# Performance work log

Measured on AMD Instinct MI355X. Metric: run time of the kernel, lower is better.

## Reference

```python
import jax, jax.numpy as jnp
import numpy as np

DIM = 128
EDGE_FEAT_DIM = 2
N_NODES = 50000
N_EDGES = 600000
EPS = 1e-5


def setup_inputs() -> dict:
    key = jax.random.key(0)
    ks = jax.random.split(key, 16)
    d = DIM
    inp = {}
    inp["x"] = jax.random.normal(ks[0], (N_NODES, d), dtype=jnp.float32)
    inp["edge_index"] = jax.random.randint(ks[1], (2, N_EDGES), 0, N_NODES, dtype=jnp.int32)
    inp["edge_weight_norm"] = jax.random.uniform(ks[2], (N_EDGES,), dtype=jnp.float32)
    inp["edge_feat"] = jax.random.normal(ks[3], (N_EDGES, EDGE_FEAT_DIM), dtype=jnp.float32)
    inp["batch"] = jnp.zeros((N_NODES,), dtype=jnp.int32)
    # phi: Linear(dim, dim)
    inp["W_phi"] = jax.random.normal(ks[4], (d, d), dtype=jnp.float32) * (1.0 / np.sqrt(d))
    inp["b_phi"] = jnp.zeros((d,), dtype=jnp.float32)
    # edge_gate: Linear(2d+2, d) -> BN(d) -> GELU -> Linear(d, 1)
    din = 2 * d + EDGE_FEAT_DIM
    inp["W_g1"] = jax.random.normal(ks[5], (din, d), dtype=jnp.float32) * (1.0 / np.sqrt(din))
    inp["b_g1"] = jnp.zeros((d,), dtype=jnp.float32)
    inp["bn_gamma"] = jnp.ones((d,), dtype=jnp.float32)
    inp["bn_beta"] = jnp.zeros((d,), dtype=jnp.float32)
    inp["bn_mean"] = jnp.zeros((d,), dtype=jnp.float32)
    inp["bn_var"] = jnp.ones((d,), dtype=jnp.float32)
    inp["W_g2"] = jax.random.normal(ks[6], (d, 1), dtype=jnp.float32) * (1.0 / np.sqrt(d))
    inp["b_g2"] = jnp.zeros((1,), dtype=jnp.float32)
    # upd: Linear(2d, d)
    inp["W_u"] = jax.random.normal(ks[7], (2 * d, d), dtype=jnp.float32) * (1.0 / np.sqrt(2 * d))
    inp["b_u"] = jnp.zeros((d,), dtype=jnp.float32)
    # LayerNorm(dim)
    inp["ln_gamma"] = jnp.ones((d,), dtype=jnp.float32)
    inp["ln_beta"] = jnp.zeros((d,), dtype=jnp.float32)
    return inp


def reference(x, edge_index, edge_weight_norm, edge_feat, batch,
              W_phi, b_phi, W_g1, b_g1, bn_gamma, bn_beta, bn_mean, bn_var,
              W_g2, b_g2, W_u, b_u, ln_gamma, ln_beta):
    src, dst = edge_index[0], edge_index[1]
    # phi(x): [N, d]
    xj = x @ W_phi + b_phi
    # edge gate MLP on [x_dst, x_src, e]: [E, 2d+2]
    g_in = jnp.concatenate([x[dst], x[src], edge_feat], axis=-1)
    h1 = g_in @ W_g1 + b_g1
    h1 = (h1 - bn_mean) * jax.lax.rsqrt(bn_var + EPS) * bn_gamma + bn_beta  # BN eval mode
    h1 = jax.nn.gelu(h1, approximate=False)
    gate = jax.nn.sigmoid(h1 @ W_g2 + b_g2)[:, 0]  # [E]
    # messages and scatter-add aggregation
    msg = xj[src] * (edge_weight_norm * gate)[:, None]  # [E, d]
    agg = jax.ops.segment_sum(msg, dst, num_segments=x.shape[0])  # [N, d]
    # update MLP + GELU + residual + LayerNorm
    h = jnp.concatenate([x, agg], axis=-1) @ W_u + b_u
    h = jax.nn.gelu(h, approximate=False)
    y = x + h
    mu = jnp.mean(y, axis=-1, keepdims=True)
    var = jnp.var(y, axis=-1, keepdims=True)
    return (y - mu) * jax.lax.rsqrt(var + EPS) * ln_gamma + ln_beta
```

## Files before the change

### kernel.cpp

```cpp
#include <hip/hip_runtime.h>
#include <hip/hip_fp16.h>
#include <math.h>

#define DIM 128
#define NN 50000
#define NE 600000
#define EPS 1e-5f
#define CAP 64

struct H8 { __half2 h[4]; };
struct F8 { float4 a, b; };

typedef _Float16 f16x8 __attribute__((ext_vector_type(8)));
typedef float    f32x4 __attribute__((ext_vector_type(4)));

__device__ __forceinline__ float gelu_fast(float x) {
    const float c1 = 2.3022085f;
    const float c2 = 0.1029437f;
    const float x2 = x * x;
    const float z  = x * __builtin_fmaf(c2, x2, c1);
    const float u  = __builtin_amdgcn_exp2f(z);
    const float r  = __builtin_amdgcn_rcpf(1.f + u);
    return __builtin_fmaf(-x, r, x);
}

__device__ __forceinline__ float sigmoid_fast(float y) {
    const float u = __builtin_amdgcn_exp2f(-1.4426950409f * y);
    return __builtin_amdgcn_rcpf(1.f + u);
}

__global__ __launch_bounds__(256) void k_prep(
    const float* __restrict__ Wg1, const float* __restrict__ bg1,
    const float* __restrict__ bng, const float* __restrict__ bnb,
    const float* __restrict__ bnm, const float* __restrict__ bnv,
    const float* __restrict__ Wphi, const float* __restrict__ bphi,
    const float* __restrict__ Wu,
    __half* __restrict__ WABth, float* __restrict__ bA,
    float* __restrict__ w0p, float* __restrict__ w1p,
    __half* __restrict__ Wct, float* __restrict__ bpu)
{
    if (blockIdx.x < 128) {
        const int k = blockIdx.x;
        const int t = threadIdx.x;
        const int c = t & 127;
        const float s = bng[c] * rsqrtf(bnv[c] + EPS);
        const float w = (t < 128) ? Wg1[k * DIM + c] : Wg1[(DIM + k) * DIM + c];
        WABth[t * DIM + k] = __float2half(w * s);
        if (k == 0 && t < 128) {
            const float tt = bnb[c] - bnm[c] * s;
            bA[c]  = bg1[c] * s + tt;
            w0p[c] = Wg1[256 * DIM + c] * s;
            w1p[c] = Wg1[257 * DIM + c] * s;
        }
    } else {
        const int a = blockIdx.x - 128;
        const int j = threadIdx.x;
        if (j < 128) {
            float acc = 0.f;
            #pragma unroll 8
            for (int k = 0; k < DIM; ++k)
                acc += Wphi[a * DIM + k] * Wu[(DIM + k) * DIM + j];
            Wct[j * 256 + a]       = __float2half(Wu[a * DIM + j]);
            Wct[j * 256 + 128 + a] = __float2half(acc);
            if (a == 0) {
                float b = 0.f;
                #pragma unroll 8
                for (int k = 0; k < DIM; ++k)
                    b += bphi[k] * Wu[(DIM + k) * DIM + j];
                bpu[j] = b;
            }
        }
    }
}

__global__ __launch_bounds__(256) void k_node_mfma(
    const float* __restrict__ x, const __half* __restrict__ WABth,
    const float* __restrict__ bA,
    __half* __restrict__ A, __half* __restrict__ Bv, __half* __restrict__ xh,
    int* __restrict__ deg)
{
    __shared__ __half xs[64][136];
    __shared__ __half ys[64][136];

    const int t    = threadIdx.x;
    const int wv   = t >> 6;
    const int lane = t & 63;
    const int n16  = lane & 15;
    const int quad = lane >> 4;
    const int m0   = blockIdx.x * 64;

    {
        const int z = blockIdx.x * 256 + t;
        if (z < NN) deg[z] = 0;
    }

    #pragma unroll
    for (int i = 0; i < 4; ++i) {
        const int idx = i * 256 + t;
        const int row = idx >> 4;
        const int col = (idx & 15) * 8;
        const int grow = min(m0 + row, NN - 1);
        const float4 xa = *(const float4*)(x + (size_t)grow * DIM + col);
        const float4 xb = *(const float4*)(x + (size_t)grow * DIM + col + 4);
        f16x8 af;
        af[0] = (_Float16)xa.x; af[1] = (_Float16)xa.y;
        af[2] = (_Float16)xa.z; af[3] = (_Float16)xa.w;
        af[4] = (_Float16)xb.x; af[5] = (_Float16)xb.y;
        af[6] = (_Float16)xb.z; af[7] = (_Float16)xb.w;
        *(f16x8*)&xs[row][col] = af;
        *(f16x8*)(xh + (size_t)grow * DIM + col) = af;
    }
    __syncthreads();

    f32x4 acc[4][4];
    #pragma unroll
    for (int mt = 0; mt < 4; ++mt)
        #pragma unroll
        for (int nt = 0; nt < 4; ++nt)
            acc[mt][nt] = (f32x4){0.f, 0.f, 0.f, 0.f};

    #pragma unroll
    for (int ks = 0; ks < 4; ++ks) {
        const int ko = ks * 32 + quad * 8;
        f16x8 bf[4];
        #pragma unroll
        for (int nt = 0; nt < 4; ++nt) {
            const int c = wv * 64 + nt * 16 + n16;
            bf[nt] = *(const f16x8*)(WABth + c * DIM + ko);
        }
        #pragma unroll
        for (int mt = 0; mt < 4; ++mt) {
            const f16x8 af = *(const f16x8*)&xs[mt * 16 + n16][ko];
            #pragma unroll
            for (int nt = 0; nt < 4; ++nt)
                acc[mt][nt] = __builtin_amdgcn_mfma_f32_16x16x32_f16(
                    af, bf[nt], acc[mt][nt], 0, 0, 0);
        }
    }
    __syncthreads();

    #pragma unroll
    for (int nt = 0; nt < 4; ++nt) {
        const int c = wv * 64 + nt * 16 + n16;
        const float bias = (c < 128) ? bA[c] : 0.f;
        #pragma unroll
        for (int mt = 0; mt < 4; ++mt)
            #pragma unroll
            for (int reg = 0; reg < 4; ++reg) {
                const int row = mt * 16 + quad * 4 + reg;
                const __half hv = __float2half(acc[mt][nt][reg] + bias);
                if (c < 128) xs[row][c]       = hv;
                else         ys[row][c - 128] = hv;
            }
    }
    __syncthreads();

    #pragma unroll
    for (int i = 0; i < 8; ++i) {
        const int chunk = t + i * 256;
        const int row = chunk >> 5;
        const int o   = (chunk & 31) * 8;
        if (m0 + row < NN) {
            if (o < 128) {
                const uint4 v = *(const uint4*)&xs[row][o];
                *(uint4*)(A + (size_t)(m0 + row) * DIM + o) = v;
            } else {
                const uint4 v = *(const uint4*)&ys[row][o - 128];
                *(uint4*)(Bv + (size_t)(m0 + row) * DIM + o - 128) = v;
            }
        }
    }
}

__global__ __launch_bounds__(256) void k_gate(
    const int*   __restrict__ ei,  const float* __restrict__ ew,
    const float* __restrict__ ef,
    const __half* __restrict__ A,  const __half* __restrict__ Bv,
    const float* __restrict__ w0p, const float* __restrict__ w1p,
    const float* __restrict__ Wg2, const float* __restrict__ bg2,
    int* __restrict__ deg, int2* __restrict__ pairs)
{
    const int t    = threadIdx.x;
    const int lane = t & 63;
    const int sub  = lane >> 4;
    const int sl   = lane & 15;
    const int c8   = sl * 8;
    const int e0   = blockIdx.x * 64 + ((t >> 6) * 4 + sub) * 4;

    const F8 WG = *(const F8*)(Wg2 + c8);
    const F8 W0 = *(const F8*)(w0p + c8);
    const F8 W1 = *(const F8*)(w1p + c8);
    const float bg2v = bg2[0];
    const float* w0 = (const float*)&W0;
    const float* w1 = (const float*)&W1;
    const float* wg = (const float*)&WG;

    const int4   srcs = *(const int4*)(ei + e0);
    const int4   dsts = *(const int4*)(ei + NE + e0);
    const float4 efA  = *(const float4*)(ef + 2 * e0);
    const float4 efB  = *(const float4*)(ef + 2 * e0 + 4);
    const float4 ewv  = *(const float4*)(ew + e0);

    const int se[4] = {srcs.x, srcs.y, srcs.z, srcs.w};
    const int de[4] = {dsts.x, dsts.y, dsts.z, dsts.w};
    const float ef0[4] = {efA.x, efA.z, efB.x, efB.z};
    const float ef1[4] = {efA.y, efA.w, efB.y, efB.w};
    const float ewe[4] = {ewv.x, ewv.y, ewv.z, ewv.w};

    H8 av[4], bv[4];
    #pragma unroll
    for (int e = 0; e < 4; ++e) {
        av[e] = *(const H8*)(A  + (size_t)de[e] * DIM + c8);
        bv[e] = *(const H8*)(Bv + (size_t)se[e] * DIM + c8);
    }

    float p[4] = {0.f, 0.f, 0.f, 0.f};
    #pragma unroll
    for (int i = 0; i < 4; ++i) {
        const int c0 = 2 * i, c1 = 2 * i + 1;
        #pragma unroll
        for (int e = 0; e < 4; ++e) {
            const float2 s = __half22float2(__hadd2(av[e].h[i], bv[e].h[i]));
            float h;
            h = s.x + ef0[e] * w0[c0] + ef1[e] * w1[c0];
            p[e] = __builtin_fmaf(gelu_fast(h), wg[c0], p[e]);
            h = s.y + ef0[e] * w0[c1] + ef1[e] * w1[c1];
            p[e] = __builtin_fmaf(gelu_fast(h), wg[c1], p[e]);
        }
    }

    #pragma unroll
    for (int off = 1; off < 16; off <<= 1) {
        #pragma unroll
        for (int e = 0; e < 4; ++e)
            p[e] += __shfl_xor(p[e], off, 64);
    }

    if (sl == 0) {
        #pragma unroll
        for (int e = 0; e < 4; ++e) {
            const float coef = ewe[e] * sigmoid_fast(p[e] + bg2v);
            const int pos = atomicAdd(&deg[de[e]], 1);
            if (pos < CAP)
                pairs[(size_t)de[e] * CAP + pos] =
                    make_int2(se[e], __float_as_int(coef));
        }
    }
}

__global__ __launch_bounds__(128, 3) void k_agg_update(
    const int* __restrict__ deg, const int2* __restrict__ pairs,
    const __half* __restrict__ xh, const __half* __restrict__ Wct,
    const float* __restrict__ bu, const float* __restrict__ bpu,
    const float* __restrict__ lng, const float* __restrict__ lnb,
    float* __restrict__ out)
{
    __shared__ __half xt[16][136];
    __shared__ __half at[2][16][136];
    __shared__ float  sct[2][16];
    __shared__ float  sred_s[2][16];
    __shared__ float  sred_ss[2][16];

    const int t    = threadIdx.x;
    const int w    = t >> 6;
    const int lane = t & 63;
    const int n16  = lane & 15;
    const int quad = lane >> 4;
    const int m0   = blockIdx.x * 16;

    const int slot = quad;
    const int sl   = n16;
    const int c8   = sl * 8;

    int    cnt[4];
    size_t pb[4];
    #pragma unroll
    for (int r = 0; r < 4; ++r) {
        const int lr = r * 4 + slot;
        const int nc = min(m0 + lr, NN - 1);
        const int d  = min(deg[nc], CAP);
        const int h  = ((d + 2) >> 2) << 1;
        const int lo = w ? h : 0;
        const int hi = w ? d : h;
        cnt[r] = hi - lo;
        pb[r]  = (size_t)nc * CAP + lo;
    }

    #pragma unroll
    for (int i = 0; i < 2; ++i) {
        const int idx = i * 128 + t;
        const int row = idx >> 4;
        const int col = (idx & 15) * 8;
        const int grow = min(m0 + row, NN - 1);
        *(f16x8*)&xt[row][col] = *(const f16x8*)(xh + (size_t)grow * DIM + col);
    }

    float acc[4][8];
    float scn[4] = {0.f, 0.f, 0.f, 0.f};
    #pragma unroll
    for (int r = 0; r < 4; ++r)
        #pragma unroll
        for (int i = 0; i < 8; ++i) acc[r][i] = 0.f;

    const int cmax = max(max(cnt[0], cnt[1]), max(cnt[2], cnt[3]));

    for (int jj = 0; jj < cmax; jj += 4) {
        int4 pq0[4], pq1[4];
        #pragma unroll
        for (int r = 0; r < 4; ++r) {
            pq0[r] = *(const int4*)(&pairs[pb[r] + jj]);
            pq1[r] = *(const int4*)(&pairs[pb[r] + jj + 2]);
        }

        int   ix[16];
        float cf[16];
        #pragma unroll
        for (int r = 0; r < 4; ++r) {
            const int q = 4 * r;
            const bool v0 = (jj     < cnt[r]);
            const bool v1 = (jj + 1 < cnt[r]);
            const bool v2 = (jj + 2 < cnt[r]);
            const bool v3 = (jj + 3 < cnt[r]);
            ix[q]     = v0 ? pq0[r].x : 0;
            cf[q]     = v0 ? __int_as_float(pq0[r].y) : 0.f;
            ix[q + 1] = v1 ? pq0[r].z : 0;
            cf[q + 1] = v1 ? __int_as_float(pq0[r].w) : 0.f;
            ix[q + 2] = v2 ? pq1[r].x : 0;
            cf[q + 2] = v2 ? __int_as_float(pq1[r].y) : 0.f;
            ix[q + 3] = v3 ? pq1[r].z : 0;
            cf[q + 3] = v3 ? __int_as_float(pq1[r].w) : 0.f;
        }

        H8 xv[16];
        #pragma unroll
        for (int q = 0; q < 16; ++q)
            xv[q] = *(const H8*)(xh + (size_t)ix[q] * DIM + c8);

        #pragma unroll
        for (int r = 0; r < 4; ++r) {
            #pragma unroll
            for (int k = 0; k < 4; ++k) {
                const int   q = 4 * r + k;
                const float c = cf[q];
                #pragma unroll
                for (int i = 0; i < 4; ++i) {
                    const float2 f = __half22float2(xv[q].h[i]);
                    acc[r][2 * i]     = __builtin_fmaf(c, f.x, acc[r][2 * i]);
                    acc[r][2 * i + 1] = __builtin_fmaf(c, f.y, acc[r][2 * i + 1]);
                }
                scn[r] += c;
            }
        }
    }

    #pragma unroll
    for (int r = 0; r < 4; ++r) {
        const int lr = r * 4 + slot;
        f16x8 hv;
        #pragma unroll
        for (int i = 0; i < 8; ++i) hv[i] = (_Float16)acc[r][i];
        *(f16x8*)&at[w][lr][c8] = hv;
        if (sl == 0) sct[w][lr] = scn[r];
    }
    __syncthreads();

    f32x4 acc2[4];
    #pragma unroll
    for (int nt = 0; nt < 4; ++nt) acc2[nt] = (f32x4){0.f, 0.f, 0.f, 0.f};

    const int rloc = n16;
    #pragma unroll
    for (int ks = 0; ks < 4; ++ks) {
        const int ko = ks * 32 + quad * 8;
        const f16x8 af = *(const f16x8*)&xt[rloc][ko];
        #pragma unroll
        for (int nt = 0; nt < 4; ++nt) {
            const int c = w * 64 + nt * 16 + n16;
            const f16x8 bf = *(const f16x8*)(Wct + c * 256 + ko);
            acc2[nt] = __builtin_amdgcn_mfma_f32_16x16x32_f16(af, bf, acc2[nt], 0, 0, 0);
        }
    }
    #pragma unroll
    for (int half = 0; half < 2; ++half) {
        #pragma unroll
        for (int ks = 0; ks < 4; ++ks) {
            const int ko = ks * 32 + quad * 8;
            const f16x8 af = *(const f16x8*)&at[half][rloc][ko];
            #pragma unroll
            for (int nt = 0; nt < 4; ++nt) {
                const int c = w * 64 + nt * 16 + n16;
                const f16x8 bf = *(const f16x8*)(Wct + c * 256 + 128 + ko);
                acc2[nt] = __builtin_amdgcn_mfma_f32_16x16x32_f16(af, bf, acc2[nt], 0, 0, 0);
            }
        }
    }

    int   rl[4];
    float scv[4];
    #pragma unroll
    for (int reg = 0; reg < 4; ++reg) {
        rl[reg]  = quad * 4 + reg;
        scv[reg] = sct[0][rl[reg]] + sct[1][rl[reg]];
    }

    float yv[4][4];
    float s[4]  = {0.f, 0.f, 0.f, 0.f};
    float ss[4] = {0.f, 0.f, 0.f, 0.f};

    #pragma unroll
    for (int nt = 0; nt < 4; ++nt) {
        const int c = w * 64 + nt * 16 + n16;
        const float buv = bu[c], bpv = bpu[c];
        #pragma unroll
        for (int reg = 0; reg < 4; ++reg) {
            float h = acc2[nt][reg] + buv + scv[reg] * bpv;
            h = gelu_fast(h);
            const float xv = __half2float(xt[rl[reg]][c]);
            const float y = xv + h;
            yv[nt][reg] = y;
            s[reg]  += y;
            ss[reg] += y * y;
        }
    }

    #pragma unroll
    for (int reg = 0; reg < 4; ++reg) {
        #pragma unroll
        for (int off = 1; off < 16; off <<= 1) {
            s[reg]  += __shfl_xor(s[reg],  off, 64);
            ss[reg] += __shfl_xor(ss[reg], off, 64);
        }
    }
    if (n16 == 0) {
        #pragma unroll
        for (int reg = 0; reg < 4; ++reg) {
            sred_s[w][rl[reg]]  = s[reg];
            sred_ss[w][rl[reg]] = ss[reg];
        }
    }
    __syncthreads();

    float mu[4], rs[4];
    #pragma unroll
    for (int reg = 0; reg < 4; ++reg) {
        const float stot  = sred_s[0][rl[reg]]  + sred_s[1][rl[reg]];
        const float sstot = sred_ss[0][rl[reg]] + sred_ss[1][rl[reg]];
        mu[reg] = stot * (1.f / DIM);
        const float var = sstot * (1.f / DIM) - mu[reg] * mu[reg];
        rs[reg] = rsqrtf(var + EPS);
    }

    #pragma unroll
    for (int nt = 0; nt < 4; ++nt) {
        const int c = w * 64 + nt * 16 + n16;
        const float gg = lng[c], bb2 = lnb[c];
        #pragma unroll
        for (int reg = 0; reg < 4; ++reg) {
            const int grow = m0 + rl[reg];
            if (grow < NN)
                __builtin_nontemporal_store(
                    (yv[nt][reg] - mu[reg]) * rs[reg] * gg + bb2,
                    &out[(size_t)grow * DIM + c]);
        }
    }
}

extern "C" void kernel_launch(void* const* d_in, const int* in_sizes, int n_in,
                              void* d_out, int out_size, void* d_ws, size_t ws_size,
                              hipStream_t stream)
{
    const float* x    = (const float*)d_in[0];
    const int*   ei   = (const int*)  d_in[1];
    const float* ew   = (const float*)d_in[2];
    const float* ef   = (const float*)d_in[3];
    const float* Wphi = (const float*)d_in[5];
    const float* bphi = (const float*)d_in[6];
    const float* Wg1  = (const float*)d_in[7];
    const float* bg1  = (const float*)d_in[8];
    const float* bng  = (const float*)d_in[9];
    const float* bnb  = (const float*)d_in[10];
    const float* bnm  = (const float*)d_in[11];
    const float* bnv  = (const float*)d_in[12];
    const float* Wg2  = (const float*)d_in[13];
    const float* bg2  = (const float*)d_in[14];
    const float* Wu   = (const float*)d_in[15];
    const float* bu   = (const float*)d_in[16];
    const float* lng  = (const float*)d_in[17];
    const float* lnb  = (const float*)d_in[18];

    float* out = (float*)d_out;

    char* wsb = (char*)d_ws;
    size_t off = 0;
    auto carve = [&](size_t bytes) -> void* {
        void* p = wsb + off;
        off += (bytes + 255) & ~(size_t)255;
        return p;
    };
    __half* xh    = (__half*)carve((size_t)NN * DIM * 2);
    __half* A     = (__half*)carve((size_t)NN * DIM * 2);
    __half* Bv    = (__half*)carve((size_t)NN * DIM * 2);
    __half* WABth = (__half*)carve(256 * DIM * 2);
    __half* Wct   = (__half*)carve(DIM * 256 * 2);
    float*  bA    = (float*) carve(DIM * 4);
    float*  w0p   = (float*) carve(DIM * 4);
    float*  w1p   = (float*) carve(DIM * 4);
    float*  bpu   = (float*) carve(DIM * 4);
    int*    deg   = (int*)   carve((size_t)NN * 4);
    int2*   pairs = (int2*)  carve((size_t)NN * CAP * 8 + 256);

    k_prep<<<256, 256, 0, stream>>>(Wg1, bg1, bng, bnb, bnm, bnv,
                                    Wphi, bphi, Wu,
                                    WABth, bA, w0p, w1p, Wct, bpu);
    k_node_mfma<<<(NN + 63) / 64, 256, 0, stream>>>(x, WABth, bA, A, Bv, xh,
                                                    deg);
    k_gate<<<NE / 64, 256, 0, stream>>>(ei, ew, ef, A, Bv, w0p, w1p, Wg2, bg2,
                                        deg, pairs);
    k_agg_update<<<(NN + 15) / 16, 128, 0, stream>>>(deg, pairs, xh, Wct,
                                                     bu, bpu, lng, lnb, out);
}
```

Baseline: 251.8 us.

## Split fused aggregate-update kernel into separate gather and MFMA update kernels

Splits the fused aggregation+update kernel into two kernels. The first is a small gather kernel with one wave per block handling four nodes, each looping over its own degree in chunks of 16 edges. It writes the fp16 aggregate and coefficient sum to a global buffer. The second kernel loads those buffers and performs the MFMA update, GELU and LayerNorm. This is meant to cut the load imbalance and low occupancy of the fused kernel's gather phase, at the cost of an extra global round-trip for the aggregate (about 12.8MB written and read) and one more kernel launch.

Result: slower. 262.7 us (+4.3%).

```diff
diff --git a/kernel.cpp b/kernel.cpp
--- a/kernel.cpp
+++ b/kernel.cpp
@@ -248,16 +248,81 @@
     }
 }
 
-__global__ __launch_bounds__(128, 3) void k_agg_update(
+__global__ __launch_bounds__(64) void k_agg(
     const int* __restrict__ deg, const int2* __restrict__ pairs,
-    const __half* __restrict__ xh, const __half* __restrict__ Wct,
+    const __half* __restrict__ xh,
+    __half* __restrict__ at_g, float* __restrict__ sc_g)
+{
+    const int t    = threadIdx.x;
+    const int slot = t >> 4;
+    const int sl   = t & 15;
+    const int c8   = sl * 8;
+    const int n    = blockIdx.x * 4 + slot;
+    const int d    = min(deg[n], CAP);
+    const size_t pb = (size_t)n * CAP;
+
+    int dmax = d;
+    dmax = max(dmax, __shfl_xor(dmax, 16, 64));
+    dmax = max(dmax, __shfl_xor(dmax, 32, 64));
+
+    float acc[8];
+    #pragma unroll
+    for (int i = 0; i < 8; ++i) acc[i] = 0.f;
+    float scn = 0.f;
+
+    for (int jj = 0; jj < dmax; jj += 16) {
+        int4 pq[8];
+        #pragma unroll
+        for (int k = 0; k < 8; ++k)
+            pq[k] = *(const int4*)(&pairs[pb + jj + 2 * k]);
+
+        int   ix[16];
+        float cf[16];
+        #pragma unroll
+        for (int k = 0; k < 8; ++k) {
+            const bool v0 = (jj + 2 * k     < d);
+            const bool v1 = (jj + 2 * k + 1 < d);
+            ix[2 * k]     = v0 ? pq[k].x : 0;
+            cf[2 * k]     = v0 ? __int_as_float(pq[k].y) : 0.f;
+            ix[2 * k + 1] = v1 ? pq[k].z : 0;
+            cf[2 * k + 1] = v1 ? __int_as_float(pq[k].w) : 0.f;
+        }
+
+        H8 xv[16];
+        #pragma unroll
+        for (int q = 0; q < 16; ++q)
+            xv[q] = *(const H8*)(xh + (size_t)ix[q] * DIM + c8);
+
+        #pragma unroll
+        for (int q = 0; q < 16; ++q) {
+            const float c = cf[q];
+            #pragma unroll
+            for (int i = 0; i < 4; ++i) {
+                const float2 f = __half22float2(xv[q].h[i]);
+                acc[2 * i]     = __builtin_fmaf(c, f.x, acc[2 * i]);
+                acc[2 * i + 1] = __builtin_fmaf(c, f.y, acc[2 * i + 1]);
+            }
+            scn += c;
+        }
+    }
+
+    f16x8 hv;
+    #pragma unroll
+    for (int i = 0; i < 8; ++i) hv[i] = (_Float16)acc[i];
+    *(f16x8*)(at_g + (size_t)n * DIM + c8) = hv;
+    if (sl == 0) sc_g[n] = scn;
+}
+
+__global__ __launch_bounds__(128) void k_upd(
+    const __half* __restrict__ xh, const __half* __restrict__ at_g,
+    const float* __restrict__ sc_g, const __half* __restrict__ Wct,
     const float* __restrict__ bu, const float* __restrict__ bpu,
     const float* __restrict__ lng, const float* __restrict__ lnb,
     float* __restrict__ out)
 {
     __shared__ __half xt[16][136];
-    __shared__ __half at[2][16][136];
-    __shared__ float  sct[2][16];
+    __shared__ __half at[16][136];
+    __shared__ float  sct[16];
     __shared__ float  sred_s[2][16];
     __shared__ float  sred_ss[2][16];
 
@@ -268,100 +333,16 @@
     const int quad = lane >> 4;
     const int m0   = blockIdx.x * 16;
 
-    const int slot = quad;
-    const int sl   = n16;
-    const int c8   = sl * 8;
-
-    int    cnt[4];
-    size_t pb[4];
-    #pragma unroll
-    for (int r = 0; r < 4; ++r) {
-        const int lr = r * 4 + slot;
-        const int nc = min(m0 + lr, NN - 1);
-        const int d  = min(deg[nc], CAP);
-        const int h  = ((d + 2) >> 2) << 1;
-        const int lo = w ? h : 0;
-        const int hi = w ? d : h;
-        cnt[r] = hi - lo;
-        pb[r]  = (size_t)nc * CAP + lo;
-    }
-
     #pragma unroll
     for (int i = 0; i < 2; ++i) {
         const int idx = i * 128 + t;
         const int row = idx >> 4;
         const int col = (idx & 15) * 8;
         const int grow = min(m0 + row, NN - 1);
-        *(f16x8*)&xt[row][col] = *(const f16x8*)(xh + (size_t)grow * DIM + col);
-    }
-
-    float acc[4][8];
-    float scn[4] = {0.f, 0.f, 0.f, 0.f};
-    #pragma unroll
-    for (int r = 0; r < 4; ++r)
-        #pragma unroll
-        for (int i = 0; i < 8; ++i) acc[r][i] = 0.f;
-
-    const int cmax = max(max(cnt[0], cnt[1]), max(cnt[2], cnt[3]));
-
-    for (int jj = 0; jj < cmax; jj += 4) {
-        int4 pq0[4], pq1[4];
-        #pragma unroll
-        for (int r = 0; r < 4; ++r) {
-            pq0[r] = *(const int4*)(&pairs[pb[r] + jj]);
-            pq1[r] = *(const int4*)(&pairs[pb[r] + jj + 2]);
-        }
-
-        int   ix[16];
-        float cf[16];
-        #pragma unroll
-        for (int r = 0; r < 4; ++r) {
-            const int q = 4 * r;
-            const bool v0 = (jj     < cnt[r]);
-            const bool v1 = (jj + 1 < cnt[r]);
-            const bool v2 = (jj + 2 < cnt[r]);
-            const bool v3 = (jj + 3 < cnt[r]);
-            ix[q]     = v0 ? pq0[r].x : 0;
-            cf[q]     = v0 ? __int_as_float(pq0[r].y) : 0.f;
-            ix[q + 1] = v1 ? pq0[r].z : 0;
-            cf[q + 1] = v1 ? __int_as_float(pq0[r].w) : 0.f;
-            ix[q + 2] = v2 ? pq1[r].x : 0;
-            cf[q + 2] = v2 ? __int_as_float(pq1[r].y) : 0.f;
-            ix[q + 3] = v3 ? pq1[r].z : 0;
-            cf[q + 3] = v3 ? __int_as_float(pq1[r].w) : 0.f;
-        }
-
-        H8 xv[16];
-        #pragma unroll
-        for (int q = 0; q < 16; ++q)
-            xv[q] = *(const H8*)(xh + (size_t)ix[q] * DIM + c8);
-
-        #pragma unroll
-        for (int r = 0; r < 4; ++r) {
-            #pragma unroll
-            for (int k = 0; k < 4; ++k) {
-                const int   q = 4 * r + k;
-                const float c = cf[q];
-                #pragma unroll
-                for (int i = 0; i < 4; ++i) {
-                    const float2 f = __half22float2(xv[q].h[i]);
-                    acc[r][2 * i]     = __builtin_fmaf(c, f.x, acc[r][2 * i]);
-                    acc[r][2 * i + 1] = __builtin_fmaf(c, f.y, acc[r][2 * i + 1]);
-                }
-                scn[r] += c;
-            }
-        }
-    }
-
-    #pragma unroll
-    for (int r = 0; r < 4; ++r) {
-        const int lr = r * 4 + slot;
-        f16x8 hv;
-        #pragma unroll
-        for (int i = 0; i < 8; ++i) hv[i] = (_Float16)acc[r][i];
-        *(f16x8*)&at[w][lr][c8] = hv;
-        if (sl == 0) sct[w][lr] = scn[r];
-    }
+        *(f16x8*)&xt[row][col] = *(const f16x8*)(xh  + (size_t)grow * DIM + col);
+        *(f16x8*)&at[row][col] = *(const f16x8*)(at_g + (size_t)grow * DIM + col);
+    }
+    if (t < 16) sct[t] = sc_g[min(m0 + t, NN - 1)];
     __syncthreads();
 
     f32x4 acc2[4];
@@ -381,17 +362,14 @@
         }
     }
     #pragma unroll
-    for (int half = 0; half < 2; ++half) {
-        #pragma unroll
-        for (int ks = 0; ks < 4; ++ks) {
-            const int ko = ks * 32 + quad * 8;
-            const f16x8 af = *(const f16x8*)&at[half][rloc][ko];
-            #pragma unroll
-            for (int nt = 0; nt < 4; ++nt) {
-                const int c = w * 64 + nt * 16 + n16;
-                const f16x8 bf = *(const f16x8*)(Wct + c * 256 + 128 + ko);
-                acc2[nt] = __builtin_amdgcn_mfma_f32_16x16x32_f16(af, bf, acc2[nt], 0, 0, 0);
-            }
+    for (int ks = 0; ks < 4; ++ks) {
+        const int ko = ks * 32 + quad * 8;
+        const f16x8 af = *(const f16x8*)&at[rloc][ko];
+        #pragma unroll
+        for (int nt = 0; nt < 4; ++nt) {
+            const int c = w * 64 + nt * 16 + n16;
+            const f16x8 bf = *(const f16x8*)(Wct + c * 256 + 128 + ko);
+            acc2[nt] = __builtin_amdgcn_mfma_f32_16x16x32_f16(af, bf, acc2[nt], 0, 0, 0);
         }
     }
 
@@ -400,7 +378,7 @@
     #pragma unroll
     for (int reg = 0; reg < 4; ++reg) {
         rl[reg]  = quad * 4 + reg;
-        scv[reg] = sct[0][rl[reg]] + sct[1][rl[reg]];
+        scv[reg] = sct[rl[reg]];
     }
 
     float yv[4][4];
@@ -500,6 +478,8 @@
     __half* xh    = (__half*)carve((size_t)NN * DIM * 2);
     __half* A     = (__half*)carve((size_t)NN * DIM * 2);
     __half* Bv    = (__half*)carve((size_t)NN * DIM * 2);
+    __half* at_g  = (__half*)carve((size_t)NN * DIM * 2);
+    float*  sc_g  = (float*) carve((size_t)NN * 4);
     __half* WABth = (__half*)carve(256 * DIM * 2);
     __half* Wct   = (__half*)carve(DIM * 256 * 2);
     float*  bA    = (float*) carve(DIM * 4);
@@ -516,6 +496,7 @@
                                                     deg);
     k_gate<<<NE / 64, 256, 0, stream>>>(ei, ew, ef, A, Bv, w0p, w1p, Wg2, bg2,
                                         deg, pairs);
-    k_agg_update<<<(NN + 15) / 16, 128, 0, stream>>>(deg, pairs, xh, Wct,
-                                                     bu, bpu, lng, lnb, out);
-}
+    k_agg<<<NN / 4, 64, 0, stream>>>(deg, pairs, xh, at_g, sc_g);
+    k_upd<<<NN / 16, 128, 0, stream>>>(xh, at_g, sc_g, Wct,
+                                       bu, bpu, lng, lnb, out);
+}
```
